# Performance work log

Measured on AMD Instinct MI355X. Metric: run time of the kernel, lower is better.

## Reference

```python
import jax, jax.numpy as jnp
import numpy as np

N = 100000      # num_nodes
E = 600000      # edges per relation
R = 3           # num_relations
F_IN = 128
F_OUT = 64


def setup_inputs() -> dict:
    key = jax.random.key(0)
    k0, k1, k2, k3 = jax.random.split(key, 4)
    x = jax.random.normal(k0, (N, F_IN), dtype=jnp.float32)
    edge_indices = jax.random.randint(k1, (R, 2, E), 0, N, dtype=jnp.int32)
    # torch.randperm per relation -> fixed permutations as int inputs
    perms = jnp.stack([jax.random.permutation(jax.random.fold_in(k2, r), N).astype(jnp.int32)
                       for r in range(R)])
    # GCNConv glorot weight + zero bias, one per relation
    Ws = jax.random.normal(k3, (R, F_IN, F_OUT), dtype=jnp.float32) * (1.0 / np.sqrt(F_IN))
    bs = jnp.zeros((R, F_OUT), dtype=jnp.float32)
    return {"x": x, "edge_indices": edge_indices, "perms": perms, "Ws": Ws, "bs": bs}


def gcn_conv(h, src, dst, W, b, n):
    """PyG GCNConv: add self-loops, sym-normalize, linear, scatter-sum, bias."""
    loops = jnp.arange(n, dtype=src.dtype)
    s = jnp.concatenate([src, loops])
    d = jnp.concatenate([dst, loops])
    deg = jax.ops.segment_sum(jnp.ones_like(s, dtype=h.dtype), d, num_segments=n)
    dinv = jnp.where(deg > 0, jax.lax.rsqrt(deg), 0.0)
    norm = dinv[s] * dinv[d]                      # [E+n]
    hw = h @ W                                    # [n, F_OUT]
    out = jax.ops.segment_sum(hw[s] * norm[:, None], d, num_segments=n)
    return out + b


def reference(x, edge_indices, perms, Ws, bs):
    # Eval mode: F.dropout(p=0.5, training=False) is identity.
    n = x.shape[0]
    pos_hs, neg_hs, summaries = [], [], []
    for r in range(R):
        src, dst = edge_indices[r, 0], edge_indices[r, 1]
        pos_h = jax.nn.relu(gcn_conv(x, src, dst, Ws[r], bs[r], n))
        neg_h = jax.nn.relu(gcn_conv(x[perms[r]], src, dst, Ws[r], bs[r], n))
        pos_hs.append(pos_h)
        neg_hs.append(neg_h)
        summaries.append(pos_h.mean(axis=0, keepdims=True))
    return (jnp.stack(pos_hs), jnp.stack(neg_hs), jnp.stack(summaries))
```

## Files before the change

### kernel.cpp

```cpp
#include <hip/hip_runtime.h>

#define F_IN 128
#define F_OUT 64
#define NCHUNK 256

typedef float f32x2 __attribute__((ext_vector_type(2)));
typedef float f32x4 __attribute__((ext_vector_type(4)));
typedef short bf16x8 __attribute__((ext_vector_type(8)));

__device__ __forceinline__ unsigned short f2bf(float f) {
    unsigned int u = __float_as_uint(f);
    u += 0x7fff + ((u >> 16) & 1);
    return (unsigned short)(u >> 16);
}
__device__ __forceinline__ float bf2f(unsigned short s) {
    return __uint_as_float((unsigned int)s << 16);
}

__global__ __launch_bounds__(256) void deg_kernel(const int* __restrict__ ei,
                                                  int* __restrict__ deg,
                                                  int N, int E) {
    int r = blockIdx.y;
    int e = blockIdx.x * 256 + threadIdx.x;
    if (e >= E) return;
    int d = ei[(size_t)r * 2 * E + E + e];
    atomicAdd(&deg[(size_t)r * N + d], 1);
}

__global__ __launch_bounds__(256) void invperm_kernel(const int* __restrict__ perm,
                                                      int* __restrict__ ip, int N) {
    int r = blockIdx.y;
    int i = blockIdx.x * 256 + threadIdx.x;
    if (i >= N) return;
    ip[(size_t)r * N + perm[(size_t)r * N + i]] = i;
}

__global__ __launch_bounds__(256) void scan_partial(const int* __restrict__ deg,
                                                    int* __restrict__ psum,
                                                    int N, int chunk) {
    int r = blockIdx.y, b = blockIdx.x;
    int start = b * chunk, end = min(start + chunk, N);
    int s = 0;
    for (int i = start + threadIdx.x; i < end; i += 256)
        s += deg[(size_t)r * N + i];
    __shared__ int ls[256];
    ls[threadIdx.x] = s;
    __syncthreads();
    for (int off = 128; off > 0; off >>= 1) {
        if (threadIdx.x < off) ls[threadIdx.x] += ls[threadIdx.x + off];
        __syncthreads();
    }
    if (threadIdx.x == 0) psum[r * NCHUNK + b] = ls[0];
}

__global__ __launch_bounds__(256) void scan_offsets(int* __restrict__ psum,
                                                    int* __restrict__ rowstart,
                                                    int N, int R) {
    int tid = threadIdx.x, lane = tid & 63, wv = tid >> 6;
    __shared__ int wsum[4];
    for (int r = 0; r < R; ++r) {
        int v = psum[r * NCHUNK + tid];
        int sc = v;
        #pragma unroll
        for (int off = 1; off < 64; off <<= 1) {
            int t = __shfl_up(sc, off, 64);
            if (lane >= off) sc += t;
        }
        if (lane == 63) wsum[wv] = sc;
        __syncthreads();
        int woff = 0;
        for (int w = 0; w < wv; ++w) woff += wsum[w];
        psum[r * NCHUNK + tid] = woff + sc - v;
        if (tid == 255) rowstart[(size_t)r * (N + 1) + N] = woff + sc;
        __syncthreads();
    }
}

__global__ __launch_bounds__(256) void scan_apply(int* __restrict__ deg,
                                                  const int* __restrict__ psum,
                                                  int* __restrict__ rowstart,
                                                  float* __restrict__ dinv,
                                                  int N, int chunk) {
    int r = blockIdx.y, b = blockIdx.x;
    int tid = threadIdx.x, lane = tid & 63, wv = tid >> 6;
    int start = b * chunk, end = min(start + chunk, N);
    int* dg = deg + (size_t)r * N;
    int* rs = rowstart + (size_t)r * (N + 1);
    float* dv = dinv + (size_t)r * N;
    __shared__ int wsum[4];
    int v[4]; int tsum = 0;
    #pragma unroll
    for (int j = 0; j < 4; ++j) {
        int idx = start + tid * 4 + j;
        v[j] = (idx < end) ? dg[idx] : 0;
        tsum += v[j];
    }
    int sc = tsum;
    #pragma unroll
    for (int off = 1; off < 64; off <<= 1) {
        int t = __shfl_up(sc, off, 64);
        if (lane >= off) sc += t;
    }
    if (lane == 63) wsum[wv] = sc;
    __syncthreads();
    int woff = 0;
    for (int w = 0; w < wv; ++w) woff += wsum[w];
    int excl = psum[r * NCHUNK + b] + woff + sc - tsum;
    #pragma unroll
    for (int j = 0; j < 4; ++j) {
        int idx = start + tid * 4 + j;
        if (idx < end) {
            rs[idx] = excl;
            dg[idx] = excl;
            dv[idx] = rsqrtf((float)(v[j] + 1));
        }
        excl += v[j];
    }
}

__global__ __launch_bounds__(256) void fill_csr(const int* __restrict__ ei,
                                                const float* __restrict__ dinv,
                                                int* __restrict__ cursor,
                                                int2* __restrict__ csr,
                                                int N, int E) {
    int r = blockIdx.y;
    int e = blockIdx.x * 256 + threadIdx.x;
    if (e >= E) return;
    const int* base = ei + (size_t)r * 2 * E;
    int s = base[e], d = base[E + e];
    const float* dv = dinv + (size_t)r * N;
    float nrm = dv[s] * dv[d];
    int pos = atomicAdd(&cursor[(size_t)r * N + d], 1);
    int2 sp; sp.x = s; sp.y = __float_as_int(nrm);
    csr[(size_t)r * E + pos] = sp;
}

__global__ __launch_bounds__(256) void w_convert(const float* __restrict__ W,
                                                 unsigned short* __restrict__ wt_hi,
                                                 unsigned short* __restrict__ wt_lo,
                                                 int R) {
    int idx = blockIdx.x * 256 + threadIdx.x;
    if (idx >= R * 64 * 128) return;
    int k = idx & 127, c = (idx >> 7) & 63, r = idx >> 13;
    float v = W[((size_t)r * F_IN + k) * F_OUT + c];
    unsigned short h = f2bf(v);
    wt_hi[idx] = h;
    wt_lo[idx] = f2bf(v - bf2f(h));
}

__global__ __launch_bounds__(256) void gemm_xw_mfma(const float* __restrict__ x,
                                                    const unsigned short* __restrict__ wt_hi,
                                                    const unsigned short* __restrict__ wt_lo,
                                                    const int* __restrict__ ip,
                                                    unsigned short* __restrict__ combined,
                                                    int N, int R) {
    constexpr int KP = 136;
    __shared__ __align__(16) unsigned short xs_hi[128 * KP];
    __shared__ __align__(16) unsigned short xs_lo[128 * KP];

    int row0 = blockIdx.x * 128;
    int tid = threadIdx.x;
    {
        int rr = tid >> 1, half = tid & 1;
        int grow = row0 + rr; if (grow >= N) grow = N - 1;
        const float* xr = x + (size_t)grow * F_IN + half * 64;
        unsigned short* dh = &xs_hi[rr * KP + half * 64];
        unsigned short* dl = &xs_lo[rr * KP + half * 64];
        #pragma unroll
        for (int c = 0; c < 64; c += 4) {
            float4 v = *(const float4*)(xr + c);
            unsigned short h0 = f2bf(v.x), h1 = f2bf(v.y),
                           h2 = f2bf(v.z), h3 = f2bf(v.w);
            ushort4 hv; hv.x = h0; hv.y = h1; hv.z = h2; hv.w = h3;
            *(ushort4*)(dh + c) = hv;
            ushort4 lv;
            lv.x = f2bf(v.x - bf2f(h0)); lv.y = f2bf(v.y - bf2f(h1));
            lv.z = f2bf(v.z - bf2f(h2)); lv.w = f2bf(v.w - bf2f(h3));
            *(ushort4*)(dl + c) = lv;
        }
    }
    __syncthreads();

    int wv = tid >> 6, lane = tid & 63;
    int l15 = lane & 15, lhi = lane >> 4;
    int nbase = wv * 32;
    for (int r = 0; r < R; ++r) {
        f32x4 acc[2][4];
        #pragma unroll
        for (int nt = 0; nt < 2; ++nt)
            #pragma unroll
            for (int ct = 0; ct < 4; ++ct)
                acc[nt][ct] = (f32x4){0.f, 0.f, 0.f, 0.f};
        const unsigned short* wh = wt_hi + (size_t)r * 64 * 128;
        const unsigned short* wl = wt_lo + (size_t)r * 64 * 128;
        #pragma unroll
        for (int kc = 0; kc < 4; ++kc) {
            int kb = kc * 32 + lhi * 8;
            bf16x8 bh[2], bl[2], ah[4], al[4];
            #pragma unroll
            for (int nt = 0; nt < 2; ++nt) {
                int ro = (nbase + nt * 16 + l15) * KP + kb;
                bh[nt] = *(const bf16x8*)&xs_hi[ro];
                bl[nt] = *(const bf16x8*)&xs_lo[ro];
            }
            #pragma unroll
            for (int ct = 0; ct < 4; ++ct) {
                int wo = (ct * 16 + l15) * 128 + kb;
                ah[ct] = *(const bf16x8*)(wh + wo);
                al[ct] = *(const bf16x8*)(wl + wo);
            }
            #pragma unroll
            for (int ct = 0; ct < 4; ++ct)
                #pragma unroll
                for (int nt = 0; nt < 2; ++nt) {
                    acc[nt][ct] = __builtin_amdgcn_mfma_f32_16x16x32_bf16(
                        ah[ct], bh[nt], acc[nt][ct], 0, 0, 0);
                    acc[nt][ct] = __builtin_amdgcn_mfma_f32_16x16x32_bf16(
                        ah[ct], bl[nt], acc[nt][ct], 0, 0, 0);
                    acc[nt][ct] = __builtin_amdgcn_mfma_f32_16x16x32_bf16(
                        al[ct], bh[nt], acc[nt][ct], 0, 0, 0);
                }
        }
        const int* ipr = ip + (size_t)r * N;
        size_t rb = (size_t)r * N;
        #pragma unroll
        for (int nt = 0; nt < 2; ++nt) {
            int xrow = row0 + nbase + nt * 16 + l15;
            if (xrow < N) {
                int nrow = ipr[xrow];
                #pragma unroll
                for (int ct = 0; ct < 4; ++ct) {
                    f32x4 a = acc[nt][ct];
                    ushort4 v;
                    v.x = f2bf(a.x); v.y = f2bf(a.y);
                    v.z = f2bf(a.z); v.w = f2bf(a.w);
                    int cb = ct * 16 + lhi * 4;
                    *(ushort4*)(combined + (rb + xrow) * 128 + cb) = v;
                    *(ushort4*)(combined + (rb + nrow) * 128 + 64 + cb) = v;
                }
            }
        }
    }
}

__global__ __launch_bounds__(256) void gather_kernel(const int2* __restrict__ csr,
                                                     const int* __restrict__ rowstart,
                                                     const float* __restrict__ dinv,
                                                     const unsigned short* __restrict__ combined,
                                                     const float* __restrict__ bs,
                                                     float* __restrict__ out_pos,
                                                     float* __restrict__ out_neg,
                                                     float* __restrict__ partial,
                                                     int N, int E) {
    int r = blockIdx.y;
    int lane = threadIdx.x & 63, wv = threadIdx.x >> 6;
    int i = blockIdx.x * 4 + wv;
    i = __builtin_amdgcn_readfirstlane(i);
    int c0 = (lane & 31) * 2;
    __shared__ float ls[4][64];
    float p0 = 0.f, p1 = 0.f;
    if (i < N) {
        const unsigned short* cw = combined + (size_t)r * N * 128;
        const int* rs = rowstart + (size_t)r * (N + 1);
        int j0 = rs[i], j1 = rs[i + 1];
        j0 = __builtin_amdgcn_readfirstlane(j0);
        j1 = __builtin_amdgcn_readfirstlane(j1);
        float di = dinv[(size_t)r * N + i];
        float w = di * di;
        unsigned int sv = *(const unsigned int*)(cw + (size_t)i * 128 + 2 * lane);
        float acc0 = bf2f((unsigned short)sv) * w;
        float acc1 = bf2f((unsigned short)(sv >> 16)) * w;
        const int2* cs = csr + (size_t)r * E;
        int last = j1 - 1;
        for (int j = j0; j < j1; j += 8) {
            int2 e[8];
            float nm[8];
            #pragma unroll
            for (int k = 0; k < 8; ++k) {
                int idx = j + k;
                int ic = idx < last ? idx : last;
                e[k] = cs[ic];
                nm[k] = (idx < j1) ? __int_as_float(e[k].y) : 0.f;
            }
            #pragma unroll
            for (int k = 0; k < 8; ++k) {
                unsigned int v = *(const unsigned int*)(cw + (size_t)e[k].x * 128 + 2 * lane);
                acc0 += bf2f((unsigned short)v) * nm[k];
                acc1 += bf2f((unsigned short)(v >> 16)) * nm[k];
            }
        }
        float2 bv = *(const float2*)(bs + r * F_OUT + c0);
        float q0 = acc0 + bv.x; q0 = q0 > 0.f ? q0 : 0.f;
        float q1 = acc1 + bv.y; q1 = q1 > 0.f ? q1 : 0.f;
        size_t off = (size_t)r * N * F_OUT + (size_t)i * F_OUT + c0;
        float* dst = (lane < 32) ? (out_pos + off) : (out_neg + off);
        f32x2 o; o.x = q0; o.y = q1;
        __builtin_nontemporal_store(o, (f32x2*)dst);
        if (lane < 32) { p0 = q0; p1 = q1; }
    }
    if (lane < 32) { ls[wv][c0] = p0; ls[wv][c0 + 1] = p1; }
    __syncthreads();
    if (wv == 0) {
        float t = ls[0][lane] + ls[1][lane] + ls[2][lane] + ls[3][lane];
        atomicAdd(&partial[((size_t)r * 256 + (blockIdx.x & 255)) * F_OUT + lane], t);
    }
}

__global__ __launch_bounds__(256) void summary_reduce(const float* __restrict__ partial,
                                                      float* __restrict__ summary,
                                                      float inv_n) {
    int r = blockIdx.x;
    int lane = threadIdx.x & 63, wv = threadIdx.x >> 6;
    __shared__ float ls[256];
    float s = 0.f;
    for (int c = wv; c < 256; c += 4)
        s += partial[((size_t)r * 256 + c) * F_OUT + lane];
    ls[threadIdx.x] = s;
    __syncthreads();
    if (wv == 0)
        summary[r * F_OUT + lane] =
            (ls[lane] + ls[64 + lane] + ls[128 + lane] + ls[192 + lane]) * inv_n;
}

extern "C" void kernel_launch(void* const* d_in, const int* in_sizes, int n_in,
                              void* d_out, int out_size, void* d_ws, size_t ws_size,
                              hipStream_t stream) {
    const float* x    = (const float*)d_in[0];
    const int*   ei   = (const int*)d_in[1];
    const int*   perm = (const int*)d_in[2];
    const float* Ws   = (const float*)d_in[3];
    const float* bs   = (const float*)d_in[4];

    const int N = in_sizes[0] / F_IN;
    const int R = in_sizes[4] / F_OUT;
    const int E = in_sizes[1] / (2 * R);

    float* out_pos = (float*)d_out;
    float* out_neg = out_pos + (size_t)R * N * F_OUT;
    float* summary = out_neg + (size_t)R * N * F_OUT;

    char* ws = (char*)d_ws;
    size_t off = 0;
    auto alloc = [&](size_t bytes) { void* p = ws + off;
        off += (bytes + 255) & ~(size_t)255; return p; };
    int*   deg      = (int*)  alloc((size_t)R * N * 4);
    float* dinv     = (float*)alloc((size_t)R * N * 4);
    int*   rowstart = (int*)  alloc((size_t)R * (N + 1) * 4);
    int*   ip       = (int*)  alloc((size_t)R * N * 4);
    int2*  csr      = (int2*) alloc((size_t)R * E * 8);
    unsigned short* combined = (unsigned short*)alloc((size_t)R * N * 128 * 2);
    float* partial  = (float*)alloc((size_t)R * 256 * F_OUT * 4);
    int*   psum     = (int*)  alloc((size_t)R * NCHUNK * 4);
    unsigned short* wt_hi = (unsigned short*)alloc((size_t)R * 64 * 128 * 2);
    unsigned short* wt_lo = (unsigned short*)alloc((size_t)R * 64 * 128 * 2);

    const int chunk = (N + NCHUNK - 1) / NCHUNK;

    hipMemsetAsync(deg, 0, (size_t)R * N * sizeof(int), stream);
    hipMemsetAsync(partial, 0, (size_t)R * 256 * F_OUT * sizeof(float), stream);

    deg_kernel<<<dim3((E + 255) / 256, R), 256, 0, stream>>>(ei, deg, N, E);
    invperm_kernel<<<dim3((N + 255) / 256, R), 256, 0, stream>>>(perm, ip, N);
    w_convert<<<(R * 64 * 128 + 255) / 256, 256, 0, stream>>>(Ws, wt_hi, wt_lo, R);
    scan_partial<<<dim3(NCHUNK, R), 256, 0, stream>>>(deg, psum, N, chunk);
    scan_offsets<<<1, 256, 0, stream>>>(psum, rowstart, N, R);
    scan_apply<<<dim3(NCHUNK, R), 256, 0, stream>>>(deg, psum, rowstart, dinv, N, chunk);
    fill_csr<<<dim3((E + 255) / 256, R), 256, 0, stream>>>(ei, dinv, deg, csr, N, E);
    gemm_xw_mfma<<<(N + 127) / 128, 256, 0, stream>>>(x, wt_hi, wt_lo, ip, combined, N, R);
    gather_kernel<<<dim3((N + 3) / 4, R), 256, 0, stream>>>(csr, rowstart, dinv,
                                                            combined, bs, out_pos,
                                                            out_neg, partial, N, E);
    summary_reduce<<<R, 256, 0, stream>>>(partial, summary, 1.0f / (float)N);
}
```

Baseline: 548.5 us.

## Merge preprocessing kernels and co-schedule CSR fill with GEMM

Fuses the degree count, inverse permutation and weight conversion into one prep kernel. The scan-offsets step is folded into scan_apply, which each block recomputes redundantly. The CSR fill and the XW GEMM become one launch whose blocks are split by index, with the GEMM tile shrunk to 64 rows so both kinds of work run at once. The two memsets are merged into one by placing the buffers next to each other. This cuts launch count and serialization, at the cost of half-size GEMM tiles that reuse each weight load over fewer rows.

```diff
diff --git a/kernel.cpp b/kernel.cpp
--- a/kernel.cpp
+++ b/kernel.cpp
@@ -17,29 +17,47 @@
     return __uint_as_float((unsigned int)s << 16);
 }
 
-__global__ __launch_bounds__(256) void deg_kernel(const int* __restrict__ ei,
-                                                  int* __restrict__ deg,
-                                                  int N, int E) {
-    int r = blockIdx.y;
-    int e = blockIdx.x * 256 + threadIdx.x;
-    if (e >= E) return;
-    int d = ei[(size_t)r * 2 * E + E + e];
-    atomicAdd(&deg[(size_t)r * N + d], 1);
-}
-
-__global__ __launch_bounds__(256) void invperm_kernel(const int* __restrict__ perm,
-                                                      int* __restrict__ ip, int N) {
-    int r = blockIdx.y;
-    int i = blockIdx.x * 256 + threadIdx.x;
-    if (i >= N) return;
-    ip[(size_t)r * N + perm[(size_t)r * N + i]] = i;
+__global__ __launch_bounds__(256) void prep_kernel(const int* __restrict__ ei,
+                                                   const int* __restrict__ perm,
+                                                   const float* __restrict__ W,
+                                                   int* __restrict__ deg,
+                                                   int* __restrict__ ip,
+                                                   unsigned short* __restrict__ wt_hi,
+                                                   unsigned short* __restrict__ wt_lo,
+                                                   int N, int E, int R,
+                                                   int degB, int invB) {
+    int b = blockIdx.x;
+    if (b < degB) {
+        int idx = b * 256 + threadIdx.x;
+        if (idx < R * E) {
+            int r = idx / E, e = idx - r * E;
+            int d = ei[(size_t)r * 2 * E + E + e];
+            atomicAdd(&deg[(size_t)r * N + d], 1);
+        }
+    } else if (b < degB + invB) {
+        int idx = (b - degB) * 256 + threadIdx.x;
+        if (idx < R * N) {
+            int r = idx / N, i = idx - r * N;
+            ip[(size_t)r * N + perm[idx]] = i;
+        }
+    } else {
+        int idx = (b - degB - invB) * 256 + threadIdx.x;
+        if (idx < R * 64 * 128) {
+            int k = idx & 127, c = (idx >> 7) & 63, r = idx >> 13;
+            float v = W[((size_t)r * F_IN + k) * F_OUT + c];
+            unsigned short h = f2bf(v);
+            wt_hi[idx] = h;
+            wt_lo[idx] = f2bf(v - bf2f(h));
+        }
+    }
 }
 
 __global__ __launch_bounds__(256) void scan_partial(const int* __restrict__ deg,
                                                     int* __restrict__ psum,
                                                     int N, int chunk) {
-    int r = blockIdx.y, b = blockIdx.x;
-    int start = b * chunk, end = min(start + chunk, N);
+    int b = blockIdx.x;
+    int r = b >> 8, c = b & 255;
+    int start = c * chunk, end = min(start + chunk, N);
     int s = 0;
     for (int i = start + threadIdx.x; i < end; i += 256)
         s += deg[(size_t)r * N + i];
@@ -50,44 +68,41 @@
         if (threadIdx.x < off) ls[threadIdx.x] += ls[threadIdx.x + off];
         __syncthreads();
     }
-    if (threadIdx.x == 0) psum[r * NCHUNK + b] = ls[0];
-}
-
-__global__ __launch_bounds__(256) void scan_offsets(int* __restrict__ psum,
-                                                    int* __restrict__ rowstart,
-                                                    int N, int R) {
+    if (threadIdx.x == 0) psum[b] = ls[0];
+}
+
+__global__ __launch_bounds__(256) void scan_apply2(int* __restrict__ deg,
+                                                   const int* __restrict__ psum,
+                                                   int* __restrict__ rowstart,
+                                                   float* __restrict__ dinv,
+                                                   int N, int chunk) {
+    int b = blockIdx.x;
+    int r = b >> 8, c = b & 255;
     int tid = threadIdx.x, lane = tid & 63, wv = tid >> 6;
+    __shared__ int incl[256];
     __shared__ int wsum[4];
-    for (int r = 0; r < R; ++r) {
-        int v = psum[r * NCHUNK + tid];
-        int sc = v;
-        #pragma unroll
-        for (int off = 1; off < 64; off <<= 1) {
-            int t = __shfl_up(sc, off, 64);
-            if (lane >= off) sc += t;
-        }
-        if (lane == 63) wsum[wv] = sc;
-        __syncthreads();
-        int woff = 0;
-        for (int w = 0; w < wv; ++w) woff += wsum[w];
-        psum[r * NCHUNK + tid] = woff + sc - v;
-        if (tid == 255) rowstart[(size_t)r * (N + 1) + N] = woff + sc;
-        __syncthreads();
-    }
-}
-
-__global__ __launch_bounds__(256) void scan_apply(int* __restrict__ deg,
-                                                  const int* __restrict__ psum,
-                                                  int* __restrict__ rowstart,
-                                                  float* __restrict__ dinv,
-                                                  int N, int chunk) {
-    int r = blockIdx.y, b = blockIdx.x;
-    int tid = threadIdx.x, lane = tid & 63, wv = tid >> 6;
-    int start = b * chunk, end = min(start + chunk, N);
+
+    int pv = psum[(r << 8) + tid];
+    int sc = pv;
+    #pragma unroll
+    for (int off = 1; off < 64; off <<= 1) {
+        int t = __shfl_up(sc, off, 64);
+        if (lane >= off) sc += t;
+    }
+    if (lane == 63) wsum[wv] = sc;
+    __syncthreads();
+    int woff = 0;
+    for (int w = 0; w < wv; ++w) woff += wsum[w];
+    incl[tid] = woff + sc;
+    __syncthreads();
+    int base = (c == 0) ? 0 : incl[c - 1];
+    if (c == 0 && tid == 0)
+        rowstart[(size_t)r * (N + 1) + N] = incl[255];
+
+    int start = c * chunk, end = min(start + chunk, N);
     int* dg = deg + (size_t)r * N;
     int* rs = rowstart + (size_t)r * (N + 1);
     float* dv = dinv + (size_t)r * N;
-    __shared__ int wsum[4];
     int v[4]; int tsum = 0;
     #pragma unroll
     for (int j = 0; j < 4; ++j) {
@@ -95,17 +110,17 @@
         v[j] = (idx < end) ? dg[idx] : 0;
         tsum += v[j];
     }
-    int sc = tsum;
+    int sc2 = tsum;
     #pragma unroll
     for (int off = 1; off < 64; off <<= 1) {
-        int t = __shfl_up(sc, off, 64);
-        if (lane >= off) sc += t;
-    }
-    if (lane == 63) wsum[wv] = sc;
-    __syncthreads();
-    int woff = 0;
-    for (int w = 0; w < wv; ++w) woff += wsum[w];
-    int excl = psum[r * NCHUNK + b] + woff + sc - tsum;
+        int t = __shfl_up(sc2, off, 64);
+        if (lane >= off) sc2 += t;
+    }
+    if (lane == 63) wsum[wv] = sc2;
+    __syncthreads();
+    int woff2 = 0;
+    for (int w = 0; w < wv; ++w) woff2 += wsum[w];
+    int excl = base + woff2 + sc2 - tsum;
     #pragma unroll
     for (int j = 0; j < 4; ++j) {
         int idx = start + tid * 4 + j;
@@ -118,56 +133,45 @@
     }
 }
 
-__global__ __launch_bounds__(256) void fill_csr(const int* __restrict__ ei,
-                                                const float* __restrict__ dinv,
-                                                int* __restrict__ cursor,
-                                                int2* __restrict__ csr,
-                                                int N, int E) {
-    int r = blockIdx.y;
-    int e = blockIdx.x * 256 + threadIdx.x;
-    if (e >= E) return;
-    const int* base = ei + (size_t)r * 2 * E;
-    int s = base[e], d = base[E + e];
-    const float* dv = dinv + (size_t)r * N;
-    float nrm = dv[s] * dv[d];
-    int pos = atomicAdd(&cursor[(size_t)r * N + d], 1);
-    int2 sp; sp.x = s; sp.y = __float_as_int(nrm);
-    csr[(size_t)r * E + pos] = sp;
-}
-
-__global__ __launch_bounds__(256) void w_convert(const float* __restrict__ W,
-                                                 unsigned short* __restrict__ wt_hi,
-                                                 unsigned short* __restrict__ wt_lo,
-                                                 int R) {
-    int idx = blockIdx.x * 256 + threadIdx.x;
-    if (idx >= R * 64 * 128) return;
-    int k = idx & 127, c = (idx >> 7) & 63, r = idx >> 13;
-    float v = W[((size_t)r * F_IN + k) * F_OUT + c];
-    unsigned short h = f2bf(v);
-    wt_hi[idx] = h;
-    wt_lo[idx] = f2bf(v - bf2f(h));
-}
-
-__global__ __launch_bounds__(256) void gemm_xw_mfma(const float* __restrict__ x,
-                                                    const unsigned short* __restrict__ wt_hi,
-                                                    const unsigned short* __restrict__ wt_lo,
-                                                    const int* __restrict__ ip,
-                                                    unsigned short* __restrict__ combined,
-                                                    int N, int R) {
+__global__ __launch_bounds__(256) void fill_gemm(const int* __restrict__ ei,
+                                                 const float* __restrict__ dinv,
+                                                 int* __restrict__ cursor,
+                                                 int2* __restrict__ csr,
+                                                 const float* __restrict__ x,
+                                                 const unsigned short* __restrict__ wt_hi,
+                                                 const unsigned short* __restrict__ wt_lo,
+                                                 const int* __restrict__ ip,
+                                                 unsigned short* __restrict__ combined,
+                                                 int N, int E, int R, int gemmB) {
     constexpr int KP = 136;
-    __shared__ __align__(16) unsigned short xs_hi[128 * KP];
-    __shared__ __align__(16) unsigned short xs_lo[128 * KP];
-
-    int row0 = blockIdx.x * 128;
+    __shared__ __align__(16) unsigned short xs_hi[64 * KP];
+    __shared__ __align__(16) unsigned short xs_lo[64 * KP];
+    int b = blockIdx.x;
+
+    if (b >= gemmB) {
+        int idx = (b - gemmB) * 256 + threadIdx.x;
+        if (idx >= R * E) return;
+        int r = idx / E, e = idx - r * E;
+        const int* base = ei + (size_t)r * 2 * E;
+        int s = base[e], d = base[E + e];
+        const float* dv = dinv + (size_t)r * N;
+        float nrm = dv[s] * dv[d];
+        int pos = atomicAdd(&cursor[(size_t)r * N + d], 1);
+        int2 sp; sp.x = s; sp.y = __float_as_int(nrm);
+        csr[(size_t)r * E + pos] = sp;
+        return;
+    }
+
+    int row0 = b * 64;
     int tid = threadIdx.x;
     {
-        int rr = tid >> 1, half = tid & 1;
+        int rr = tid >> 2, q = tid & 3;
         int grow = row0 + rr; if (grow >= N) grow = N - 1;
-        const float* xr = x + (size_t)grow * F_IN + half * 64;
-        unsigned short* dh = &xs_hi[rr * KP + half * 64];
-        unsigned short* dl = &xs_lo[rr * KP + half * 64];
+        const float* xr = x + (size_t)grow * F_IN + q * 32;
+        unsigned short* dh = &xs_hi[rr * KP + q * 32];
+        unsigned short* dl = &xs_lo[rr * KP + q * 32];
         #pragma unroll
-        for (int c = 0; c < 64; c += 4) {
+        for (int c = 0; c < 32; c += 4) {
             float4 v = *(const float4*)(xr + c);
             unsigned short h0 = f2bf(v.x), h1 = f2bf(v.y),
                            h2 = f2bf(v.z), h3 = f2bf(v.w);
@@ -183,26 +187,20 @@
 
     int wv = tid >> 6, lane = tid & 63;
     int l15 = lane & 15, lhi = lane >> 4;
-    int nbase = wv * 32;
+    int nbase = wv * 16;
     for (int r = 0; r < R; ++r) {
-        f32x4 acc[2][4];
+        f32x4 acc[4];
         #pragma unroll
-        for (int nt = 0; nt < 2; ++nt)
-            #pragma unroll
-            for (int ct = 0; ct < 4; ++ct)
-                acc[nt][ct] = (f32x4){0.f, 0.f, 0.f, 0.f};
+        for (int ct = 0; ct < 4; ++ct) acc[ct] = (f32x4){0.f, 0.f, 0.f, 0.f};
         const unsigned short* wh = wt_hi + (size_t)r * 64 * 128;
         const unsigned short* wl = wt_lo + (size_t)r * 64 * 128;
         #pragma unroll
         for (int kc = 0; kc < 4; ++kc) {
             int kb = kc * 32 + lhi * 8;
-            bf16x8 bh[2], bl[2], ah[4], al[4];
-            #pragma unroll
-            for (int nt = 0; nt < 2; ++nt) {
-                int ro = (nbase + nt * 16 + l15) * KP + kb;
-                bh[nt] = *(const bf16x8*)&xs_hi[ro];
-                bl[nt] = *(const bf16x8*)&xs_lo[ro];
-            }
+            int ro = (nbase + l15) * KP + kb;
+            bf16x8 bh = *(const bf16x8*)&xs_hi[ro];
+            bf16x8 bl = *(const bf16x8*)&xs_lo[ro];
+            bf16x8 ah[4], al[4];
             #pragma unroll
             for (int ct = 0; ct < 4; ++ct) {
                 int wo = (ct * 16 + l15) * 128 + kb;
@@ -210,34 +208,26 @@
                 al[ct] = *(const bf16x8*)(wl + wo);
             }
             #pragma unroll
-            for (int ct = 0; ct < 4; ++ct)
-                #pragma unroll
-                for (int nt = 0; nt < 2; ++nt) {
-                    acc[nt][ct] = __builtin_amdgcn_mfma_f32_16x16x32_bf16(
-                        ah[ct], bh[nt], acc[nt][ct], 0, 0, 0);
-                    acc[nt][ct] = __builtin_amdgcn_mfma_f32_16x16x32_bf16(
-                        ah[ct], bl[nt], acc[nt][ct], 0, 0, 0);
-                    acc[nt][ct] = __builtin_amdgcn_mfma_f32_16x16x32_bf16(
-                        al[ct], bh[nt], acc[nt][ct], 0, 0, 0);
-                }
+            for (int ct = 0; ct < 4; ++ct) {
+                acc[ct] = __builtin_amdgcn_mfma_f32_16x16x32_bf16(ah[ct], bh, acc[ct], 0, 0, 0);
+                acc[ct] = __builtin_amdgcn_mfma_f32_16x16x32_bf16(ah[ct], bl, acc[ct], 0, 0, 0);
+                acc[ct] = __builtin_amdgcn_mfma_f32_16x16x32_bf16(al[ct], bh, acc[ct], 0, 0, 0);
+            }
         }
         const int* ipr = ip + (size_t)r * N;
         size_t rb = (size_t)r * N;
-        #pragma unroll
-        for (int nt = 0; nt < 2; ++nt) {
-            int xrow = row0 + nbase + nt * 16 + l15;
-            if (xrow < N) {
-                int nrow = ipr[xrow];
-                #pragma unroll
-                for (int ct = 0; ct < 4; ++ct) {
-                    f32x4 a = acc[nt][ct];
-                    ushort4 v;
-                    v.x = f2bf(a.x); v.y = f2bf(a.y);
-                    v.z = f2bf(a.z); v.w = f2bf(a.w);
-                    int cb = ct * 16 + lhi * 4;
-                    *(ushort4*)(combined + (rb + xrow) * 128 + cb) = v;
-                    *(ushort4*)(combined + (rb + nrow) * 128 + 64 + cb) = v;
-                }
+        int xrow = row0 + nbase + l15;
+        if (xrow < N) {
+            int nrow = ipr[xrow];
+            #pragma unroll
+            for (int ct = 0; ct < 4; ++ct) {
+                f32x4 a = acc[ct];
+                ushort4 v;
+                v.x = f2bf(a.x); v.y = f2bf(a.y);
+                v.z = f2bf(a.z); v.w = f2bf(a.w);
+                int cb = ct * 16 + lhi * 4;
+                *(ushort4*)(combined + (rb + xrow) * 128 + cb) = v;
+                *(ushort4*)(combined + (rb + nrow) * 128 + 64 + cb) = v;
             }
         }
     }
@@ -344,29 +334,32 @@
     auto alloc = [&](size_t bytes) { void* p = ws + off;
         off += (bytes + 255) & ~(size_t)255; return p; };
     int*   deg      = (int*)  alloc((size_t)R * N * 4);
+    float* partial  = (float*)alloc((size_t)R * 256 * F_OUT * 4);
     float* dinv     = (float*)alloc((size_t)R * N * 4);
     int*   rowstart = (int*)  alloc((size_t)R * (N + 1) * 4);
     int*   ip       = (int*)  alloc((size_t)R * N * 4);
     int2*  csr      = (int2*) alloc((size_t)R * E * 8);
     unsigned short* combined = (unsigned short*)alloc((size_t)R * N * 128 * 2);
-    float* partial  = (float*)alloc((size_t)R * 256 * F_OUT * 4);
     int*   psum     = (int*)  alloc((size_t)R * NCHUNK * 4);
     unsigned short* wt_hi = (unsigned short*)alloc((size_t)R * 64 * 128 * 2);
     unsigned short* wt_lo = (unsigned short*)alloc((size_t)R * 64 * 128 * 2);
 
     const int chunk = (N + NCHUNK - 1) / NCHUNK;
-
-    hipMemsetAsync(deg, 0, (size_t)R * N * sizeof(int), stream);
-    hipMemsetAsync(partial, 0, (size_t)R * 256 * F_OUT * sizeof(float), stream);
-
-    deg_kernel<<<dim3((E + 255) / 256, R), 256, 0, stream>>>(ei, deg, N, E);
-    invperm_kernel<<<dim3((N + 255) / 256, R), 256, 0, stream>>>(perm, ip, N);
-    w_convert<<<(R * 64 * 128 + 255) / 256, 256, 0, stream>>>(Ws, wt_hi, wt_lo, R);
-    scan_partial<<<dim3(NCHUNK, R), 256, 0, stream>>>(deg, psum, N, chunk);
-    scan_offsets<<<1, 256, 0, stream>>>(psum, rowstart, N, R);
-    scan_apply<<<dim3(NCHUNK, R), 256, 0, stream>>>(deg, psum, rowstart, dinv, N, chunk);
-    fill_csr<<<dim3((E + 255) / 256, R), 256, 0, stream>>>(ei, dinv, deg, csr, N, E);
-    gemm_xw_mfma<<<(N + 127) / 128, 256, 0, stream>>>(x, wt_hi, wt_lo, ip, combined, N, R);
+    const int degB = (R * E + 255) / 256;
+    const int invB = (R * N + 255) / 256;
+    const int wB   = (R * 64 * 128 + 255) / 256;
+    const int gemmB = (N + 63) / 64;
+
+    size_t zbytes = (size_t)((char*)dinv - (char*)deg);
+    hipMemsetAsync(deg, 0, zbytes, stream);
+
+    prep_kernel<<<degB + invB + wB, 256, 0, stream>>>(ei, perm, Ws, deg, ip,
+                                                      wt_hi, wt_lo, N, E, R,
+                                                      degB, invB);
+    scan_partial<<<R * NCHUNK, 256, 0, stream>>>(deg, psum, N, chunk);
+    scan_apply2<<<R * NCHUNK, 256, 0, stream>>>(deg, psum, rowstart, dinv, N, chunk);
+    fill_gemm<<<gemmB + degB, 256, 0, stream>>>(ei, dinv, deg, csr, x, wt_hi,
+                                                wt_lo, ip, combined, N, E, R, gemmB);
     gather_kernel<<<dim3((N + 3) / 4, R), 256, 0, stream>>>(csr, rowstart, dinv,
                                                             combined, bs, out_pos,
                                                             out_neg, partial, N, E);
```

Measured after the change: 544.2 us. No clear change (-0.8%).
